# Optimization experiments

Measured on AMD Instinct MI355X. Metric: run time of the kernel, lower is better.

The kernel has to match this reference:

```python
import jax, jax.numpy as jnp
import numpy as np

RADIUS = 4.0
NS = 4      # num_samples
SUB = 2     # subsampling

def sqdist(a, b):
    # a [B,M,3], b [B,N,3] -> squared dists [B,M,N]
    return jnp.sum((a[:, :, None, :] - b[:, None, :, :]) ** 2, axis=-1)

def furthest_point_sample(xyz, npoint):
    # xyz [B,N,3] -> idx [B,npoint]; matches CUDA FPS (starts at index 0)
    B, N, _ = xyz.shape
    barange = jnp.arange(B)
    def step(carry, _):
        dists, last = carry
        lastp = xyz[barange, last][:, None, :]          # [B,1,3]
        d = jnp.sum((xyz - lastp) ** 2, axis=-1)        # [B,N]
        dists = jnp.minimum(dists, d)
        nxt = jnp.argmax(dists, axis=1).astype(jnp.int32)
        return (dists, nxt), last
    init = (jnp.full((B, N), 1e10, xyz.dtype), jnp.zeros((B,), jnp.int32))
    _, idxs = jax.lax.scan(step, init, None, length=npoint)
    return jnp.transpose(idxs)                          # [B,npoint]

def gather_points(xyz, idx):
    # xyz [B,N,3], idx [B,M] -> [B,M,3]
    return jax.vmap(lambda x, i: x[i])(xyz, idx)

def group(features, idx):
    # features [B,C,N], idx [B,M,S] -> [B,C,M,S]
    return jax.vmap(lambda f, i: f[:, i])(features, idx)

def ball_query(radius, nsample, xyz, new_xyz):
    # first nsample points of xyz (by index order) within radius of each center,
    # slots padded with the first found neighbor (0 if none) - CUDA ball_query semantics
    N = xyz.shape[1]
    d2 = sqdist(new_xyz, xyz)                                  # [B,M,N]
    order = jnp.where(d2 < radius * radius, jnp.arange(N)[None, None, :], N)
    idx = jnp.sort(order, axis=-1)[..., :nsample]
    first = idx[..., :1]
    idx = jnp.where(idx == N, first, idx)
    return jnp.where(idx == N, 0, idx).astype(jnp.int32)

def point_rnn_cell(P1, X1, state, W, radius, nsample, out_ch):
    # P1 [B,M,3]; X1 [B,Cin,M] or None; W [Cout, Cin+Cout+3]
    B, M, _ = P1.shape
    if state is None:
        P2 = jnp.zeros((B, M, 3), P1.dtype)
        S2 = jnp.zeros((B, out_ch, M), P1.dtype)
    else:
        P2, S2 = state
    idx = ball_query(radius, nsample, P2, P1)                  # [B,M,S]
    P2g = group(jnp.transpose(P2, (0, 2, 1)), idx)             # [B,3,M,S]
    S2g = group(S2, idx)                                       # [B,Cout,M,S]
    disp = P2g - jnp.transpose(P1, (0, 2, 1))[..., None]
    if X1 is None:
        corr = jnp.concatenate([S2g, disp], axis=1)
    else:
        X1e = jnp.broadcast_to(X1[..., None], X1.shape + (nsample,))
        corr = jnp.concatenate([S2g, X1e, disp], axis=1)
    S1 = jnp.max(jnp.einsum('oc,bcms->boms', W, corr), axis=3)  # 1x1 conv, no bias, then max-pool
    return (P1, S1)

def query_group_max(radius, nsample, xyz, new_xyz, features):
    # QueryAndGroup(use_xyz=False) followed by max over neighbors
    idx = ball_query(radius, nsample, xyz, new_xyz)
    return jnp.max(group(features, idx), axis=-1)              # [B,C,M]

def three_interpolate(unknown, known, known_feats):
    # 3-NN inverse-(squared)-distance interpolation; PointnetFPModule(mlp=[128]) has no conv layers
    d2 = sqdist(unknown, known)                                # [B,n,m]
    negd, idx = jax.lax.top_k(-d2, 3)                          # 3 smallest squared dists
    recip = 1.0 / (-negd + 1e-8)
    w = recip / jnp.sum(recip, axis=-1, keepdims=True)         # [B,n,3]
    gf = group(known_feats, idx)                               # [B,C,n,3]
    return jnp.sum(gf * w[:, None, :, :], axis=-1)             # [B,C,n]

def run_step(frame, states, W1, W2, W3, N):
    N1, N2, N3 = N // SUB, N // SUB ** 2, N // SUB ** 3
    xyz1 = gather_points(frame, furthest_point_sample(frame, N1))
    s1 = point_rnn_cell(xyz1, None, states[0], W1, 1 * RADIUS + 1e-6, 3 * NS, 64)
    xyz2 = gather_points(s1[0], furthest_point_sample(s1[0], N2))
    feat2 = query_group_max(2 * RADIUS / 4 + 1e-6, NS, s1[0], xyz2, s1[1])
    s2 = point_rnn_cell(xyz2, feat2, states[1], W2, 2 * RADIUS + 1e-6, 2 * NS, 128)
    xyz3 = gather_points(s2[0], furthest_point_sample(s2[0], N3))
    feat3 = query_group_max(4 * RADIUS / 4 + 1e-6, NS, s2[0], xyz3, s2[1])
    s3 = point_rnn_cell(xyz3, feat3, states[2], W3, 3 * RADIUS + 1e-6, 1 * NS, 256)
    return (s1, s2, s3)

def setup_inputs() -> dict:
    key = jax.random.key(0)
    ks = jax.random.split(key, 12)
    B, L, N = 4, 8, 2048
    sc = 0.05
    return {
        'xyzs': jax.random.normal(ks[0], (B, L, N, 3), jnp.float32),
        'en_w1': jax.random.normal(ks[1], (64, 67), jnp.float32) * sc,
        'en_w2': jax.random.normal(ks[2], (128, 195), jnp.float32) * sc,
        'en_w3': jax.random.normal(ks[3], (256, 387), jnp.float32) * sc,
        'de_w1': jax.random.normal(ks[4], (64, 67), jnp.float32) * sc,
        'de_w2': jax.random.normal(ks[5], (128, 195), jnp.float32) * sc,
        'de_w3': jax.random.normal(ks[6], (256, 387), jnp.float32) * sc,
        'mlp_w1': jax.random.normal(ks[7], (64, 448), jnp.float32) * sc,
        'mlp_b1': jax.random.normal(ks[8], (64,), jnp.float32) * sc,
        'mlp_w2': jax.random.normal(ks[9], (3, 64), jnp.float32) * sc,
        'mlp_b2': jax.random.normal(ks[10], (3,), jnp.float32) * sc,
    }

def reference(xyzs, en_w1, en_w2, en_w3, de_w1, de_w2, de_w3, mlp_w1, mlp_b1, mlp_w2, mlp_b2):
    B, L, N, _ = xyzs.shape
    states = (None, None, None)
    # encoder over first L/2 frames
    for t in range(L // 2):
        states = run_step(xyzs[:, t], states, en_w1, en_w2, en_w3, N)
    frame = xyzs[:, L // 2 - 1]
    preds = []
    for t in range(L // 2, L):
        states = run_step(frame, states, de_w1, de_w2, de_w3, N)
        (p1, f1), (p2, f2), (p3, f3) = states
        l3 = jnp.concatenate([three_interpolate(p2, p3, f3), f2], axis=1)   # [B,384,N2]
        l2 = jnp.concatenate([three_interpolate(p1, p2, l3), f1], axis=1)   # [B,448,N1]
        l1 = three_interpolate(frame, p1, l2)                               # [B,448,N]
        h = jax.nn.relu(jnp.einsum('oc,bcn->bon', mlp_w1, l1) + mlp_b1[None, :, None])
        motion = jnp.einsum('oc,bcn->bon', mlp_w2, h) + mlp_b2[None, :, None]
        motion = jnp.transpose(motion, (0, 2, 1))                           # [B,N,3]
        frame = frame + motion
        preds.append(frame)
    return jnp.stack(preds, axis=1)                                          # [B,L/2,N,3]
```

## Files before the change

kernel.cpp:

```cpp
#include <hip/hip_runtime.h>

static constexpr int B  = 4;
static constexpr int N0 = 2048;
static constexpr int LF = 8;
static constexpr int M1 = 1024, M2 = 512, M3 = 256;
static constexpr int O1 = 64, O2 = 128, O3 = 256;
static constexpr int NS1 = 12, NS2 = 8, NS3 = 4, NSQ = 4;
static constexpr int C1 = 67, C2 = 195, C3 = 387;
static constexpr int C41 = 68, C42 = 196, C43 = 388;
static constexpr long XS = 3 * (long)M1;

static constexpr int WP_E1 = 0;
static constexpr int WP_E2 = 4352;
static constexpr int WP_E3 = 29440;
static constexpr int WP_D1 = 128768;
static constexpr int WP_D2 = 133120;
static constexpr int WP_D3 = 158208;
static constexpr int WP_M1 = 257536;
static constexpr int WP_TOT = 286208;

__device__ __forceinline__ float sq3(float ax, float ay, float az,
                                     float bx, float by, float bz) {
  float dx = __fsub_rn(ax, bx), dy = __fsub_rn(ay, by), dz = __fsub_rn(az, bz);
  return __fadd_rn(__fadd_rn(__fmul_rn(dx, dx), __fmul_rn(dy, dy)),
                   __fmul_rn(dz, dz));
}

template <int CTRL>
__device__ __forceinline__ int dpp_i(int v) {
  return __builtin_amdgcn_update_dpp(v, v, CTRL, 0xf, 0xf, false);
}
template <int CTRL>
__device__ __forceinline__ float dpp_maxf(float m) {
  const float o = __uint_as_float((unsigned)dpp_i<CTRL>((int)__float_as_uint(m)));
  return fmaxf(m, o);
}
template <int CTRL>
__device__ __forceinline__ unsigned dpp_minu(unsigned v) {
  const unsigned o = (unsigned)dpp_i<CTRL>((int)v);
  return o < v ? o : v;
}
template <int CTRL>
__device__ __forceinline__ void dpp_min64_step(unsigned& hi, unsigned& lo) {
  const unsigned ohi = (unsigned)dpp_i<CTRL>((int)hi);
  const unsigned olo = (unsigned)dpp_i<CTRL>((int)lo);
  const bool take = (ohi < hi) || (ohi == hi && olo < lo);
  hi = take ? ohi : hi;
  lo = take ? olo : lo;
}

__device__ __forceinline__ float4 wsum3(float4 a, float4 b, float4 c,
                                        float w0, float w1, float w2) {
  float4 r;
  r.x = __fadd_rn(__fadd_rn(__fmul_rn(a.x, w0), __fmul_rn(b.x, w1)), __fmul_rn(c.x, w2));
  r.y = __fadd_rn(__fadd_rn(__fmul_rn(a.y, w0), __fmul_rn(b.y, w1)), __fmul_rn(c.y, w2));
  r.z = __fadd_rn(__fadd_rn(__fmul_rn(a.z, w0), __fmul_rn(b.z, w1)), __fmul_rn(c.z, w2));
  r.w = __fadd_rn(__fadd_rn(__fmul_rn(a.w, w0), __fmul_rn(b.w, w1)), __fmul_rn(c.w, w2));
  return r;
}

__global__ __launch_bounds__(256) void pack_w(
    const float* __restrict__ e1, const float* __restrict__ e2,
    const float* __restrict__ e3, const float* __restrict__ d1,
    const float* __restrict__ d2, const float* __restrict__ d3,
    const float* __restrict__ m1, float* __restrict__ dst) {
  int t = blockIdx.x * 256 + threadIdx.x;
  const float* src; int C, O; long dof;
  if (t < 4288) { src = e1; C = C1; O = O1; dof = WP_E1; }
  else if (t < 29248) { src = e2; C = C2; O = O2; dof = WP_E2; t -= 4288; }
  else if (t < 128320) { src = e3; C = C3; O = O3; dof = WP_E3; t -= 29248; }
  else if (t < 132608) { src = d1; C = C1; O = O1; dof = WP_D1; t -= 128320; }
  else if (t < 157568) { src = d2; C = C2; O = O2; dof = WP_D2; t -= 132608; }
  else if (t < 256640) { src = d3; C = C3; O = O3; dof = WP_D3; t -= 157568; }
  else if (t < 285312) { src = m1; C = 448; O = 64; dof = WP_M1; t -= 256640; }
  else return;
  const int o = t / C, c = t - o * C;
  dst[dof + ((long)(c >> 2) * O + o) * 4 + (c & 3)] = src[t];
}

template <int N, int NPOINT>
__global__ __launch_bounds__(256, 1) void fps8(const float* __restrict__ pts,
                                               long s1, long s2,
                                               float* __restrict__ out,
                                               long o1, long o2,
                                               const float* __restrict__ cfsrc,
                                               float* __restrict__ cfdst,
                                               int copy_y) {
  if ((int)blockIdx.y == copy_y) {
    const int b = blockIdx.x;
    for (int e = threadIdx.x; e < N0 * 3; e += 256)
      cfdst[(long)b * N0 * 3 + e] = cfsrc[((long)b * LF + (LF / 2 - 1)) * N0 * 3 + e];
    return;
  }
  constexpr int K = N / 256;
  const float* p = pts + (long)blockIdx.x * s1 + (long)blockIdx.y * s2;
  float* outb = out + (long)blockIdx.x * o1 + (long)blockIdx.y * o2;
  const int tid = threadIdx.x;
  const int lane = tid & 63;
  const int wid = tid >> 6;
  __shared__ float4 sp[N];
  __shared__ float sel[NPOINT * 3];
  __shared__ unsigned long long wbest[2][4];
  float ppx[K], ppy[K], ppz[K], dist[K];
#pragma unroll
  for (int k = 0; k < K; ++k) {
    const int j = k * 256 + tid;
    const float x = p[3 * j + 0], y = p[3 * j + 1], z = p[3 * j + 2];
    ppx[k] = x; ppy[k] = y; ppz[k] = z;
    sp[j] = make_float4(x, y, z, 0.f);
    dist[k] = 1e10f;
  }
  __syncthreads();
  const float4 c0 = sp[0];
  float lx = c0.x, ly = c0.y, lz = c0.z;
  for (int i = 0; i < NPOINT; ++i) {
    if (tid == 0) {
      sel[3 * i + 0] = lx; sel[3 * i + 1] = ly; sel[3 * i + 2] = lz;
    }
    float bdm = 0.f;
    int bk = 0;
#pragma unroll
    for (int k = 0; k < K; ++k) {
      const float d = sq3(ppx[k], ppy[k], ppz[k], lx, ly, lz);
      const float dm = fminf(dist[k], d);
      dist[k] = dm;
      const bool take = dm > bdm;
      bdm = take ? dm : bdm;
      bk = take ? k : bk;
    }
    float mx = bdm;
    mx = dpp_maxf<0x111>(mx);
    mx = dpp_maxf<0x112>(mx);
    mx = dpp_maxf<0x114>(mx);
    mx = dpp_maxf<0x118>(mx);
    mx = dpp_maxf<0x142>(mx);
    mx = dpp_maxf<0x143>(mx);
    const float wmax = __uint_as_float(
        (unsigned)__builtin_amdgcn_readlane((int)__float_as_uint(mx), 63));
    unsigned cand = (bdm == wmax) ? (unsigned)((bk << 8) + tid) : 0xFFFFFFFFu;
    cand = dpp_minu<0x111>(cand);
    cand = dpp_minu<0x112>(cand);
    cand = dpp_minu<0x114>(cand);
    cand = dpp_minu<0x118>(cand);
    cand = dpp_minu<0x142>(cand);
    cand = dpp_minu<0x143>(cand);
    const unsigned minj = (unsigned)__builtin_amdgcn_readlane((int)cand, 63);
    if (lane == 63)
      wbest[i & 1][wid] =
          ((unsigned long long)__float_as_uint(wmax) << 32) | (2047u - minj);
    __syncthreads();
    unsigned long long gk = 0ull;
#pragma unroll
    for (int w = 0; w < 4; ++w) {
      const unsigned long long e = wbest[i & 1][w];
      gk = (e > gk) ? e : gk;
    }
    const int gidx = 2047 - (int)(gk & 0x7FFull);
    const float4 c = sp[gidx];
    lx = c.x; ly = c.y; lz = c.z;
  }
  __syncthreads();
  for (int e = tid; e < NPOINT * 3; e += 256) outb[e] = sel[e];
}

template <int NS>
__device__ __forceinline__ void wave_bq(float qx, float qy, float qz,
                                        const float* __restrict__ src, int Ns,
                                        float r2, int* __restrict__ sidx, int lane) {
  int cnt = 0;
  for (int base = 0; base < Ns && cnt < NS; base += 64) {
    const int j = base + lane;
    bool in = false;
    if (j < Ns)
      in = sq3(qx, qy, qz, src[3 * j], src[3 * j + 1], src[3 * j + 2]) < r2;
    const unsigned long long mask = __ballot(in);
    const int pos = cnt + (int)__popcll(mask & ((1ull << lane) - 1ull));
    if (in && pos < NS) sidx[pos] = j;
    cnt += (int)__popcll(mask);
  }
  const int cc = cnt < NS ? cnt : NS;
  const int fill = (cc > 0) ? sidx[0] : 0;
  if (lane >= cc && lane < NS) sidx[lane] = fill;
}

struct FusedArgs {
  int n1, n2, n3, nk;
  const float *c1_xc, *c1_xp, *c1_W, *c1_Sp; float* c1_Sc;
  const float *c2_xc, *c2_xp, *c2_W, *c2_Sp, *c2_S1; float* c2_Sc;
  const float *c3_xc, *c3_xp, *c3_W, *c3_Sp, *c3_S2; float* c3_Sc;
  const float *k_xc, *k_frame;
  int *ii2, *ii1, *ii0;
  float *iw2, *iw1, *iw0;
  float r2c1, r2c2, r2q2, r2c3, r2q3;
};

__global__ __launch_bounds__(256) void fused_cells(FusedArgs a) {
  __shared__ __align__(16) float smem[3312];
  const int tid = threadIdx.x;
  const int lane = tid & 63;
  const int wave = tid >> 6;
  int bid = blockIdx.x;

  if (bid < a.n1) {
    float* corr2 = smem + (size_t)wave * 828;
    int* sidx = (int*)(corr2 + 816);
    const int u = bid * 4 + wave;
    const int b = u >> 10, m = u & (M1 - 1);
    const float* p1 = a.c1_xc + (long)b * XS + 3 * m;
    const float p1x = p1[0], p1y = p1[1], p1z = p1[2];
    const float* p2b = a.c1_xp + (long)b * XS;
    wave_bq<NS1>(p1x, p1y, p1z, p2b, M1, a.r2c1, sidx, lane);
    __builtin_amdgcn_wave_barrier();
    for (int e = lane; e < NS1 * C41; e += 64) {
      const int s = e / C41, c = e - s * C41;
      const int j = sidx[s];
      float v;
      if (c < O1) {
        v = a.c1_Sp[((long)b * M1 + j) * O1 + c];
      } else if (c < C1) {
        const int d = c - O1;
        v = __fsub_rn(p2b[3 * j + d], (d == 0) ? p1x : ((d == 1) ? p1y : p1z));
      } else {
        v = 0.f;
      }
      corr2[e] = v;
    }
    __builtin_amdgcn_wave_barrier();
    const float4* wp4 = (const float4*)a.c1_W;
    float accs[NS1];
#pragma unroll
    for (int s = 0; s < NS1; ++s) accs[s] = 0.f;
    for (int q = 0; q < C41 / 4; ++q) {
      const float4 wv = wp4[(long)q * O1 + lane];
#pragma unroll
      for (int s = 0; s < NS1; ++s) {
        const float4 cv = *(const float4*)(corr2 + s * C41 + 4 * q);
        float acc = accs[s];
        acc = fmaf(wv.x, cv.x, acc);
        acc = fmaf(wv.y, cv.y, acc);
        acc = fmaf(wv.z, cv.z, acc);
        acc = fmaf(wv.w, cv.w, acc);
        accs[s] = acc;
      }
    }
    float best = accs[0];
#pragma unroll
    for (int s = 1; s < NS1; ++s) best = fmaxf(best, accs[s]);
    a.c1_Sc[((long)b * M1 + m) * O1 + lane] = best;
    return;
  }
  bid -= a.n1;

  if (bid < a.n2) {
    const int half = tid >> 7;
    const int ht = tid & 127;
    const int hw = (tid >> 6) & 1;
    float* base = smem + (size_t)half * 1644;
    float* corr2 = base;
    int* sidx = (int*)(base + 1568);
    int* sfidx = (int*)(base + 1576);
    float* feat = base + 1580;
    const int u = bid * 2 + half;
    const int b = u >> 9, m = u & (M2 - 1);
    const float* p1 = a.c2_xc + (long)b * XS + 3 * m;
    const float p1x = p1[0], p1y = p1[1], p1z = p1[2];
    const float* p2b = a.c2_xp + (long)b * XS;
    if (hw == 0)
      wave_bq<NS2>(p1x, p1y, p1z, p2b, M2, a.r2c2, sidx, lane);
    else
      wave_bq<NSQ>(p1x, p1y, p1z, a.c2_xc + (long)b * XS, M1, a.r2q2, sfidx, lane);
    __syncthreads();
    if (ht < O1) {
      float bv = -3.0e38f;
#pragma unroll
      for (int s = 0; s < NSQ; ++s)
        bv = fmaxf(bv, a.c2_S1[((long)b * M1 + sfidx[s]) * O1 + ht]);
      feat[ht] = bv;
    }
    __syncthreads();
    for (int e = ht; e < NS2 * C42; e += 128) {
      const int s = e / C42, c = e - s * C42;
      const int j = sidx[s];
      float v;
      if (c < O2) {
        v = a.c2_Sp[((long)b * M2 + j) * O2 + c];
      } else if (c < O2 + O1) {
        v = feat[c - O2];
      } else if (c < C2) {
        const int d = c - O2 - O1;
        v = __fsub_rn(p2b[3 * j + d], (d == 0) ? p1x : ((d == 1) ? p1y : p1z));
      } else {
        v = 0.f;
      }
      corr2[e] = v;
    }
    __syncthreads();
    const float4* wp4 = (const float4*)a.c2_W;
    float accs[NS2];
#pragma unroll
    for (int s = 0; s < NS2; ++s) accs[s] = 0.f;
    for (int q = 0; q < C42 / 4; ++q) {
      const float4 wv = wp4[(long)q * O2 + ht];
#pragma unroll
      for (int s = 0; s < NS2; ++s) {
        const float4 cv = *(const float4*)(corr2 + s * C42 + 4 * q);
        float acc = accs[s];
        acc = fmaf(wv.x, cv.x, acc);
        acc = fmaf(wv.y, cv.y, acc);
        acc = fmaf(wv.z, cv.z, acc);
        acc = fmaf(wv.w, cv.w, acc);
        accs[s] = acc;
      }
    }
    float best = accs[0];
#pragma unroll
    for (int s = 1; s < NS2; ++s) best = fmaxf(best, accs[s]);
    a.c2_Sc[((long)b * M2 + m) * O2 + ht] = best;
    return;
  }
  bid -= a.n2;

  if (bid < a.n3) {
    float* corr2 = smem;
    int* sidx = (int*)(smem + 1552);
    int* sfidx = (int*)(smem + 1556);
    float* feat = smem + 1560;
    const int b = bid >> 8, m = bid & (M3 - 1);
    const float* p1 = a.c3_xc + (long)b * XS + 3 * m;
    const float p1x = p1[0], p1y = p1[1], p1z = p1[2];
    const float* p2b = a.c3_xp + (long)b * XS;
    if (wave == 0)
      wave_bq<NS3>(p1x, p1y, p1z, p2b, M3, a.r2c3, sidx, lane);
    else if (wave == 1)
      wave_bq<NSQ>(p1x, p1y, p1z, a.c3_xc + (long)b * XS, M2, a.r2q3, sfidx, lane);
    __syncthreads();
    if (tid < O2) {
      float bv = -3.0e38f;
#pragma unroll
      for (int s = 0; s < NSQ; ++s)
        bv = fmaxf(bv, a.c3_S2[((long)b * M2 + sfidx[s]) * O2 + tid]);
      feat[tid] = bv;
    }
    __syncthreads();
    for (int e = tid; e < NS3 * C43; e += 256) {
      const int s = e / C43, c = e - s * C43;
      const int j = sidx[s];
      float v;
      if (c < O3) {
        v = a.c3_Sp[((long)b * M3 + j) * O3 + c];
      } else if (c < O3 + O2) {
        v = feat[c - O3];
      } else if (c < C3) {
        const int d = c - O3 - O2;
        v = __fsub_rn(p2b[3 * j + d], (d == 0) ? p1x : ((d == 1) ? p1y : p1z));
      } else {
        v = 0.f;
      }
      corr2[e] = v;
    }
    __syncthreads();
    const float4* wp4 = (const float4*)a.c3_W;
    float accs[NS3];
#pragma unroll
    for (int s = 0; s < NS3; ++s) accs[s] = 0.f;
    for (int q = 0; q < C43 / 4; ++q) {
      const float4 wv = wp4[(long)q * O3 + tid];
#pragma unroll
      for (int s = 0; s < NS3; ++s) {
        const float4 cv = *(const float4*)(corr2 + s * C43 + 4 * q);
        float acc = accs[s];
        acc = fmaf(wv.x, cv.x, acc);
        acc = fmaf(wv.y, cv.y, acc);
        acc = fmaf(wv.z, cv.z, acc);
        acc = fmaf(wv.w, cv.w, acc);
        accs[s] = acc;
      }
    }
    float best = accs[0];
#pragma unroll
    for (int s = 1; s < NS3; ++s) best = fmaxf(best, accs[s]);
    a.c3_Sc[((long)b * M3 + m) * O3 + tid] = best;
    return;
  }
  bid -= a.n3;

  {
    int q, Mu, Mk;
    const float* unk; long ustr; int* oi; float* ow;
    if (bid < 512) {
      q = bid * 4 + wave; Mu = M2; Mk = M3; unk = a.k_xc; ustr = XS;
      oi = a.ii2; ow = a.iw2;
    } else if (bid < 1536) {
      q = (bid - 512) * 4 + wave; Mu = M1; Mk = M2; unk = a.k_xc; ustr = XS;
      oi = a.ii1; ow = a.iw1;
    } else {
      q = (bid - 1536) * 4 + wave; Mu = N0; Mk = M1; unk = a.k_frame; ustr = 3L * N0;
      oi = a.ii0; ow = a.iw0;
    }
    const int b = q / Mu, m = q - b * Mu;
    const float* qq = unk + (long)b * ustr + (long)m * 3;
    const float qx = qq[0], qy = qq[1], qz = qq[2];
    const float* s = a.k_xc + (long)b * XS;
    unsigned long long k0 = ~0ull, k1 = ~0ull, k2 = ~0ull;
    const int steps = Mk >> 6;
    for (int t7 = 0; t7 < steps; ++t7) {
      const int j = (t7 << 6) + lane;
      const float dd = sq3(qx, qy, qz, s[3 * j], s[3 * j + 1], s[3 * j + 2]);
      const unsigned long long key =
          ((unsigned long long)__float_as_uint(dd) << 32) | (unsigned)j;
      if (key < k0) { k2 = k1; k1 = k0; k0 = key; }
      else if (key < k1) { k2 = k1; k1 = key; }
      else if (key < k2) { k2 = key; }
    }
    float dw[3]; int jw[3];
#pragma unroll
    for (int r = 0; r < 3; ++r) {
      unsigned mhi = (unsigned)(k0 >> 32), mlo = (unsigned)k0;
      dpp_min64_step<0x111>(mhi, mlo);
      dpp_min64_step<0x112>(mhi, mlo);
      dpp_min64_step<0x114>(mhi, mlo);
      dpp_min64_step<0x118>(mhi, mlo);
      dpp_min64_step<0x142>(mhi, mlo);
      dpp_min64_step<0x143>(mhi, mlo);
      const unsigned whi = (unsigned)__builtin_amdgcn_readlane((int)mhi, 63);
      const unsigned wlo = (unsigned)__builtin_amdgcn_readlane((int)mlo, 63);
      const unsigned long long w = ((unsigned long long)whi << 32) | wlo;
      dw[r] = __uint_as_float(whi);
      jw[r] = (int)wlo;
      if (k0 == w) { k0 = k1; k1 = k2; k2 = ~0ull; }
    }
    const float r0 = 1.0f / __fadd_rn(dw[0], 1e-8f);
    const float r1 = 1.0f / __fadd_rn(dw[1], 1e-8f);
    const float r2 = 1.0f / __fadd_rn(dw[2], 1e-8f);
    const float sum = __fadd_rn(__fadd_rn(r0, r1), r2);
    if (lane == 0) {
      ow[q * 3 + 0] = r0 / sum;
      ow[q * 3 + 1] = r1 / sum;
      ow[q * 3 + 2] = r2 / sum;
      oi[q * 3 + 0] = jw[0];
      oi[q * 3 + 1] = jw[1];
      oi[q * 3 + 2] = jw[2];
    }
  }
}

__global__ __launch_bounds__(256) void buildl2_kernel(const float* __restrict__ S3c,
                                                      const float* __restrict__ S2c,
                                                      const float* __restrict__ S1c,
                                                      const int* __restrict__ ii1,
                                                      const float* __restrict__ iw1,
                                                      const int* __restrict__ ii2,
                                                      const float* __restrict__ iw2,
                                                      float* __restrict__ l2) {
  const int t = blockIdx.x * 256 + threadIdx.x;
  const int bm = t / 112;
  const int c0 = (t - bm * 112) * 4;
  const int b = bm >> 10;
  const int* id1 = ii1 + (long)bm * 3;
  const float* w1 = iw1 + (long)bm * 3;
  float4 v;
  if (c0 < O3) {
    float4 v2[3];
#pragma unroll
    for (int k = 0; k < 3; ++k) {
      const int m2 = id1[k];
      const int* id2 = ii2 + ((long)b * M2 + m2) * 3;
      const float* w2 = iw2 + ((long)b * M2 + m2) * 3;
      const float4 s0 = *(const float4*)(S3c + ((long)b * M3 + id2[0]) * O3 + c0);
      const float4 s1 = *(const float4*)(S3c + ((long)b * M3 + id2[1]) * O3 + c0);
      const float4 s2 = *(const float4*)(S3c + ((long)b * M3 + id2[2]) * O3 + c0);
      v2[k] = wsum3(s0, s1, s2, w2[0], w2[1], w2[2]);
    }
    v = wsum3(v2[0], v2[1], v2[2], w1[0], w1[1], w1[2]);
  } else if (c0 < 384) {
    const int cc = c0 - O3;
    const float4 s0 = *(const float4*)(S2c + ((long)b * M2 + id1[0]) * O2 + cc);
    const float4 s1 = *(const float4*)(S2c + ((long)b * M2 + id1[1]) * O2 + cc);
    const float4 s2 = *(const float4*)(S2c + ((long)b * M2 + id1[2]) * O2 + cc);
    v = wsum3(s0, s1, s2, w1[0], w1[1], w1[2]);
  } else {
    v = *(const float4*)(S1c + (long)bm * O1 + (c0 - 384));
  }
  *(float4*)(l2 + (long)bm * 448 + c0) = v;
}

__global__ __launch_bounds__(256) void mlp_kernel(const float* __restrict__ l2,
                                                  const int* __restrict__ ii,
                                                  const float* __restrict__ iw,
                                                  const float* __restrict__ W1P,
                                                  const float* __restrict__ b1,
                                                  const float* __restrict__ W2,
                                                  const float* __restrict__ b2,
                                                  float* __restrict__ frame,
                                                  float* __restrict__ out, int td) {
  __shared__ __align__(16) float smem[4 * 512];
  const int lane = threadIdx.x & 63;
  const int wave = threadIdx.x >> 6;
  float* col = smem + (size_t)wave * 512;
  float* h = col + 448;
  const int u = blockIdx.x * 4 + wave;
  const int b = u >> 11, n = u & (N0 - 1);
  const int* id = ii + (long)u * 3;
  const float* w = iw + (long)u * 3;
  const float w0 = w[0], w1 = w[1], w2v = w[2];
  const float4* r0 = (const float4*)(l2 + ((long)b * M1 + id[0]) * 448);
  const float4* r1 = (const float4*)(l2 + ((long)b * M1 + id[1]) * 448);
  const float4* r2 = (const float4*)(l2 + ((long)b * M1 + id[2]) * 448);
  float4* col4 = (float4*)col;
  for (int q = lane; q < 112; q += 64)
    col4[q] = wsum3(r0[q], r1[q], r2[q], w0, w1, w2v);
  __builtin_amdgcn_wave_barrier();
  const float4* wp4 = (const float4*)W1P;
  float acc = b1[lane];
  for (int q = 0; q < 112; ++q) {
    const float4 wv = wp4[(long)q * 64 + lane];
    const float4 cv = col4[q];
    acc = fmaf(wv.x, cv.x, acc);
    acc = fmaf(wv.y, cv.y, acc);
    acc = fmaf(wv.z, cv.z, acc);
    acc = fmaf(wv.w, cv.w, acc);
  }
  h[lane] = fmaxf(acc, 0.0f);
  __builtin_amdgcn_wave_barrier();
  if (lane < 3) {
    const float* w2r = W2 + lane * 64;
    float acc2 = b2[lane];
    for (int c = 0; c < 64; ++c) acc2 = fmaf(w2r[c], h[c], acc2);
    const float nf = frame[(long)u * 3 + lane] + acc2;
    frame[(long)u * 3 + lane] = nf;
    out[(((long)b * 4 + td) * N0 + n) * 3 + lane] = nf;
  }
}

extern "C" void kernel_launch(void* const* d_in, const int* in_sizes, int n_in,
                              void* d_out, int out_size, void* d_ws, size_t ws_size,
                              hipStream_t stream) {
  const float* xyzs = (const float*)d_in[0];
  const float* enw[3] = {(const float*)d_in[1], (const float*)d_in[2], (const float*)d_in[3]};
  const float* dew[3] = {(const float*)d_in[4], (const float*)d_in[5], (const float*)d_in[6]};
  const float* mw1 = (const float*)d_in[7];
  const float* mb1 = (const float*)d_in[8];
  const float* mw2 = (const float*)d_in[9];
  const float* mb2 = (const float*)d_in[10];
  float* out = (float*)d_out;

  float* ws = (float*)d_ws;
  size_t off = 0;
  auto alloc = [&](size_t nn) { float* p = ws + off; off += nn; return p; };
  const long st1 = (long)B * M1 * 3;
  float* frame = alloc((size_t)B * N0 * 3);
  float* xyz1e = alloc((size_t)4 * st1);
  float* xyz1d[2] = {alloc((size_t)st1), alloc((size_t)st1)};
  float* z1 = alloc((size_t)st1);
  float* S1bf[2] = {alloc((size_t)B * O1 * M1), alloc((size_t)B * O1 * M1)};
  float* S2bf[2] = {alloc((size_t)B * O2 * M2), alloc((size_t)B * O2 * M2)};
  float* S3bf[2] = {alloc((size_t)B * O3 * M3), alloc((size_t)B * O3 * M3)};
  float* l2 = alloc((size_t)B * 448 * M1);
  float* iw0 = alloc((size_t)B * N0 * 3);
  int* ii0 = (int*)alloc((size_t)B * N0 * 3);
  float* iw1 = alloc((size_t)B * M1 * 3);
  int* ii1 = (int*)alloc((size_t)B * M1 * 3);
  float* iw2 = alloc((size_t)B * M2 * 3);
  int* ii2 = (int*)alloc((size_t)B * M2 * 3);
  float* wt = alloc((size_t)WP_TOT);

  hipMemsetAsync(z1, 0, (size_t)st1 * 4, stream);
  hipMemsetAsync(S1bf[1], 0, (size_t)B * O1 * M1 * 4, stream);
  hipMemsetAsync(S2bf[1], 0, (size_t)B * O2 * M2 * 4, stream);
  hipMemsetAsync(S3bf[1], 0, (size_t)B * O3 * M3 * 4, stream);
  hipMemsetAsync(wt, 0, (size_t)WP_TOT * 4, stream);

  double r;
  r = 4.0 + 1e-6;             const float r2c1 = (float)(r * r);
  r = 2.0 * 4.0 / 4.0 + 1e-6; const float r2q2 = (float)(r * r);
  r = 2.0 * 4.0 + 1e-6;       const float r2c2 = (float)(r * r);
  r = 4.0 * 4.0 / 4.0 + 1e-6; const float r2q3 = (float)(r * r);
  r = 3.0 * 4.0 + 1e-6;       const float r2c3 = (float)(r * r);

  pack_w<<<dim3((285312 + 255) / 256), 256, 0, stream>>>(
      enw[0], enw[1], enw[2], dew[0], dew[1], dew[2], mw1, wt);

  fps8<2048, 1024><<<dim3(B, 5), 256, 0, stream>>>(xyzs, (long)LF * N0 * 3,
                                                   (long)N0 * 3, xyz1e, XS, st1,
                                                   xyzs, frame, 4);

  const float* x1_of_t[LF] = {
      xyz1e + 0 * st1, xyz1e + 1 * st1, xyz1e + 2 * st1, xyz1e + 3 * st1,
      xyz1e + 3 * st1, xyz1d[0], xyz1d[1], xyz1d[0]};

  const float* wp1[2] = {wt + WP_E1, wt + WP_D1};
  const float* wp2[2] = {wt + WP_E2, wt + WP_D2};
  const float* wp3[2] = {wt + WP_E3, wt + WP_D3};

  auto launch_fused = [&](int t1, int t2, int t3, int tk) {
    FusedArgs a{};
    int nb = 0;
    if (t1 >= 0) {
      a.n1 = B * M1 / 4;
      a.c1_xc = x1_of_t[t1];
      a.c1_xp = (t1 == 0) ? z1 : x1_of_t[t1 - 1];
      a.c1_W = wp1[t1 >= 4];
      a.c1_Sp = S1bf[1 - (t1 & 1)];
      a.c1_Sc = S1bf[t1 & 1];
      nb += a.n1;
    }
    if (t2 >= 0) {
      a.n2 = B * M2 / 2;
      a.c2_xc = x1_of_t[t2];
      a.c2_xp = (t2 == 0) ? z1 : x1_of_t[t2 - 1];
      a.c2_W = wp2[t2 >= 4];
      a.c2_Sp = S2bf[1 - (t2 & 1)];
      a.c2_S1 = S1bf[t2 & 1];
      a.c2_Sc = S2bf[t2 & 1];
      nb += a.n2;
    }
    if (t3 >= 0) {
      a.n3 = B * M3;
      a.c3_xc = x1_of_t[t3];
      a.c3_xp = (t3 == 0) ? z1 : x1_of_t[t3 - 1];
      a.c3_W = wp3[t3 >= 4];
      a.c3_Sp = S3bf[1 - (t3 & 1)];
      a.c3_S2 = S2bf[t3 & 1];
      a.c3_Sc = S3bf[t3 & 1];
      nb += a.n3;
    }
    if (tk >= 0) {
      a.nk = 3584;
      a.k_xc = x1_of_t[tk];
      a.k_frame = frame;
      a.ii2 = ii2; a.ii1 = ii1; a.ii0 = ii0;
      a.iw2 = iw2; a.iw1 = iw1; a.iw0 = iw0;
      nb += a.nk;
    }
    a.r2c1 = r2c1; a.r2c2 = r2c2; a.r2q2 = r2q2; a.r2c3 = r2c3; a.r2q3 = r2q3;
    fused_cells<<<dim3((unsigned)nb), 256, 0, stream>>>(a);
  };

  auto tail = [&](int t) {
    buildl2_kernel<<<dim3(B * M1 * 112 / 256), 256, 0, stream>>>(
        S3bf[t & 1], S2bf[t & 1], S1bf[t & 1], ii1, iw1, ii2, iw2, l2);
    mlp_kernel<<<dim3(B * N0 / 4), 256, 0, stream>>>(
        l2, ii0, iw0, wt + WP_M1, mb1, mw2, mb2, frame, out, t - 4);
  };

  launch_fused(0, -1, -1, -1);
  launch_fused(1, 0, -1, -1);
  launch_fused(2, 1, 0, -1);
  launch_fused(3, 2, 1, -1);
  launch_fused(4, 3, 2, 4);
  launch_fused(-1, 4, 3, -1);
  launch_fused(-1, -1, 4, -1);
  tail(4);

  for (int t = 5; t < LF; ++t) {
    fps8<2048, 1024><<<dim3(B, 1), 256, 0, stream>>>(frame, (long)N0 * 3, 0,
                                                     (float*)x1_of_t[t], XS, 0,
                                                     nullptr, nullptr, -1);
    launch_fused(t, -1, -1, t);
    launch_fused(-1, t, -1, -1);
    launch_fused(-1, -1, t, -1);
    tail(t);
  }
  (void)in_sizes; (void)n_in; (void)out_size; (void)ws_size;
}
```

Before: 2.775 ms.

## Select two FPS points per iteration using top-3 candidate speculation

Rewrites furthest point sampling so each iteration keeps a per-thread top-3 of (distance, index) keys, reduces them across waves, and when the second candidate stays farther than the third after accounting for distance to the first pick, commits both points in one round. This aims to halve the number of block-wide barriers and serial reduction rounds in the FPS loop, which is latency-bound. In exchange each round does more work: a 64-bit three-pass DPP reduction, a top-3 insertion per element and a cross-wave merge. The exactness argument depends on the top-3 test matching sequential argmax with its tie-breaking, so results could drift.

```diff
diff --git a/kernel.cpp b/kernel.cpp
--- a/kernel.cpp
+++ b/kernel.cpp
@@ -31,14 +31,12 @@
   return __builtin_amdgcn_update_dpp(v, v, CTRL, 0xf, 0xf, false);
 }
 template <int CTRL>
-__device__ __forceinline__ float dpp_maxf(float m) {
-  const float o = __uint_as_float((unsigned)dpp_i<CTRL>((int)__float_as_uint(m)));
-  return fmaxf(m, o);
-}
-template <int CTRL>
-__device__ __forceinline__ unsigned dpp_minu(unsigned v) {
-  const unsigned o = (unsigned)dpp_i<CTRL>((int)v);
-  return o < v ? o : v;
+__device__ __forceinline__ void dpp_max_step(unsigned& hi, unsigned& lo) {
+  const unsigned ohi = (unsigned)dpp_i<CTRL>((int)hi);
+  const unsigned olo = (unsigned)dpp_i<CTRL>((int)lo);
+  const bool take = (ohi > hi) || (ohi == hi && olo > lo);
+  hi = take ? ohi : hi;
+  lo = take ? olo : lo;
 }
 template <int CTRL>
 __device__ __forceinline__ void dpp_min64_step(unsigned& hi, unsigned& lo) {
@@ -79,7 +77,7 @@
 }
 
 template <int N, int NPOINT>
-__global__ __launch_bounds__(256, 1) void fps8(const float* __restrict__ pts,
+__global__ __launch_bounds__(256, 1) void fps9(const float* __restrict__ pts,
                                                long s1, long s2,
                                                float* __restrict__ out,
                                                long o1, long o2,
@@ -100,7 +98,7 @@
   const int wid = tid >> 6;
   __shared__ float4 sp[N];
   __shared__ float sel[NPOINT * 3];
-  __shared__ unsigned long long wbest[2][4];
+  __shared__ unsigned long long wsl[2][4][3];
   float ppx[K], ppy[K], ppz[K], dist[K];
 #pragma unroll
   for (int k = 0; k < K; ++k) {
@@ -112,52 +110,104 @@
   }
   __syncthreads();
   const float4 c0 = sp[0];
-  float lx = c0.x, ly = c0.y, lz = c0.z;
-  for (int i = 0; i < NPOINT; ++i) {
+  float p1x = c0.x, p1y = c0.y, p1z = c0.z;
+  float p2x = c0.x, p2y = c0.y, p2z = c0.z;
+  int pend2 = 0;
+  int cnt = 0, r = 0;
+  while (true) {
     if (tid == 0) {
-      sel[3 * i + 0] = lx; sel[3 * i + 1] = ly; sel[3 * i + 2] = lz;
-    }
-    float bdm = 0.f;
-    int bk = 0;
-#pragma unroll
-    for (int k = 0; k < K; ++k) {
-      const float d = sq3(ppx[k], ppy[k], ppz[k], lx, ly, lz);
-      const float dm = fminf(dist[k], d);
-      dist[k] = dm;
-      const bool take = dm > bdm;
-      bdm = take ? dm : bdm;
-      bk = take ? k : bk;
-    }
-    float mx = bdm;
-    mx = dpp_maxf<0x111>(mx);
-    mx = dpp_maxf<0x112>(mx);
-    mx = dpp_maxf<0x114>(mx);
-    mx = dpp_maxf<0x118>(mx);
-    mx = dpp_maxf<0x142>(mx);
-    mx = dpp_maxf<0x143>(mx);
-    const float wmax = __uint_as_float(
-        (unsigned)__builtin_amdgcn_readlane((int)__float_as_uint(mx), 63));
-    unsigned cand = (bdm == wmax) ? (unsigned)((bk << 8) + tid) : 0xFFFFFFFFu;
-    cand = dpp_minu<0x111>(cand);
-    cand = dpp_minu<0x112>(cand);
-    cand = dpp_minu<0x114>(cand);
-    cand = dpp_minu<0x118>(cand);
-    cand = dpp_minu<0x142>(cand);
-    cand = dpp_minu<0x143>(cand);
-    const unsigned minj = (unsigned)__builtin_amdgcn_readlane((int)cand, 63);
-    if (lane == 63)
-      wbest[i & 1][wid] =
-          ((unsigned long long)__float_as_uint(wmax) << 32) | (2047u - minj);
+      sel[3 * cnt + 0] = p1x; sel[3 * cnt + 1] = p1y; sel[3 * cnt + 2] = p1z;
+      if (pend2) {
+        sel[3 * cnt + 3] = p2x; sel[3 * cnt + 4] = p2y; sel[3 * cnt + 5] = p2z;
+      }
+    }
+    cnt += 1 + pend2;
+    if (cnt >= NPOINT) break;
+    unsigned long long K0 = 0ull, K1 = 0ull, K2 = 0ull;
+    if (pend2) {
+#pragma unroll
+      for (int k = 0; k < K; ++k) {
+        const float d1 = sq3(ppx[k], ppy[k], ppz[k], p1x, p1y, p1z);
+        float dm = fminf(dist[k], d1);
+        const float d2 = sq3(ppx[k], ppy[k], ppz[k], p2x, p2y, p2z);
+        dm = fminf(dm, d2);
+        dist[k] = dm;
+        const unsigned long long key =
+            ((unsigned long long)__float_as_uint(dm) << 32) |
+            (unsigned)(2047 - (k * 256 + tid));
+        if (key > K0) { K2 = K1; K1 = K0; K0 = key; }
+        else if (key > K1) { K2 = K1; K1 = key; }
+        else if (key > K2) { K2 = key; }
+      }
+    } else {
+#pragma unroll
+      for (int k = 0; k < K; ++k) {
+        const float d1 = sq3(ppx[k], ppy[k], ppz[k], p1x, p1y, p1z);
+        const float dm = fminf(dist[k], d1);
+        dist[k] = dm;
+        const unsigned long long key =
+            ((unsigned long long)__float_as_uint(dm) << 32) |
+            (unsigned)(2047 - (k * 256 + tid));
+        if (key > K0) { K2 = K1; K1 = K0; K0 = key; }
+        else if (key > K1) { K2 = K1; K1 = key; }
+        else if (key > K2) { K2 = key; }
+      }
+    }
+    unsigned long long wv0, wv1, wv2;
+#pragma unroll
+    for (int e = 0; e < 3; ++e) {
+      unsigned hi = (unsigned)(K0 >> 32), lo = (unsigned)K0;
+      dpp_max_step<0x111>(hi, lo);
+      dpp_max_step<0x112>(hi, lo);
+      dpp_max_step<0x114>(hi, lo);
+      dpp_max_step<0x118>(hi, lo);
+      dpp_max_step<0x142>(hi, lo);
+      dpp_max_step<0x143>(hi, lo);
+      const unsigned whi = (unsigned)__builtin_amdgcn_readlane((int)hi, 63);
+      const unsigned wlo = (unsigned)__builtin_amdgcn_readlane((int)lo, 63);
+      const unsigned long long wm = ((unsigned long long)whi << 32) | wlo;
+      if (e == 0) wv0 = wm; else if (e == 1) wv1 = wm; else wv2 = wm;
+      if (K0 == wm) { K0 = K1; K1 = K2; K2 = 0ull; }
+    }
+    if (lane == 63) {
+      wsl[r & 1][wid][0] = wv0;
+      wsl[r & 1][wid][1] = wv1;
+      wsl[r & 1][wid][2] = wv2;
+    }
     __syncthreads();
-    unsigned long long gk = 0ull;
-#pragma unroll
-    for (int w = 0; w < 4; ++w) {
-      const unsigned long long e = wbest[i & 1][w];
-      gk = (e > gk) ? e : gk;
-    }
-    const int gidx = 2047 - (int)(gk & 0x7FFull);
-    const float4 c = sp[gidx];
-    lx = c.x; ly = c.y; lz = c.z;
+    unsigned long long t00 = wsl[r & 1][0][0], t01 = wsl[r & 1][0][1], t02 = wsl[r & 1][0][2];
+    unsigned long long t10 = wsl[r & 1][1][0], t11 = wsl[r & 1][1][1], t12 = wsl[r & 1][1][2];
+    unsigned long long t20 = wsl[r & 1][2][0], t21 = wsl[r & 1][2][1], t22 = wsl[r & 1][2][2];
+    unsigned long long t30 = wsl[r & 1][3][0], t31 = wsl[r & 1][3][1], t32 = wsl[r & 1][3][2];
+    int l0 = 0, l1 = 0, l2 = 0, l3 = 0;
+    unsigned long long G0, G1, G2;
+#pragma unroll
+    for (int pass = 0; pass < 3; ++pass) {
+      const unsigned long long h0 = (l0 == 0) ? t00 : (l0 == 1) ? t01 : (l0 == 2) ? t02 : 0ull;
+      const unsigned long long h1 = (l1 == 0) ? t10 : (l1 == 1) ? t11 : (l1 == 2) ? t12 : 0ull;
+      const unsigned long long h2 = (l2 == 0) ? t20 : (l2 == 1) ? t21 : (l2 == 2) ? t22 : 0ull;
+      const unsigned long long h3 = (l3 == 0) ? t30 : (l3 == 1) ? t31 : (l3 == 2) ? t32 : 0ull;
+      const unsigned long long m01 = h0 > h1 ? h0 : h1;
+      const unsigned long long m23 = h2 > h3 ? h2 : h3;
+      const unsigned long long g = m01 > m23 ? m01 : m23;
+      if (pass == 0) G0 = g; else if (pass == 1) G1 = g; else G2 = g;
+      l0 += (h0 == g); l1 += (h1 == g); l2 += (h2 == g); l3 += (h3 == g);
+    }
+    const int g1 = 2047 - (int)(G0 & 0x7FFull);
+    const int g2 = 2047 - (int)(G1 & 0x7FFull);
+    const float4 cc1 = sp[g1];
+    const float4 cc2 = sp[g2];
+    const float v2 = __uint_as_float((unsigned)(G1 >> 32));
+    const float v3 = __uint_as_float((unsigned)(G2 >> 32));
+    const float d21 = sq3(cc2.x, cc2.y, cc2.z, cc1.x, cc1.y, cc1.z);
+    const float v2p = fminf(v2, d21);
+    const bool take2 = (v2p > v3) && (cnt + 2 <= NPOINT);
+    p1x = cc1.x; p1y = cc1.y; p1z = cc1.z;
+    p2x = take2 ? cc2.x : cc1.x;
+    p2y = take2 ? cc2.y : cc1.y;
+    p2z = take2 ? cc2.z : cc1.z;
+    pend2 = take2 ? 1 : 0;
+    ++r;
   }
   __syncthreads();
   for (int e = tid; e < NPOINT * 3; e += 256) outb[e] = sel[e];
@@ -580,7 +630,7 @@
   pack_w<<<dim3((285312 + 255) / 256), 256, 0, stream>>>(
       enw[0], enw[1], enw[2], dew[0], dew[1], dew[2], mw1, wt);
 
-  fps8<2048, 1024><<<dim3(B, 5), 256, 0, stream>>>(xyzs, (long)LF * N0 * 3,
+  fps9<2048, 1024><<<dim3(B, 5), 256, 0, stream>>>(xyzs, (long)LF * N0 * 3,
                                                    (long)N0 * 3, xyz1e, XS, st1,
                                                    xyzs, frame, 4);
 
@@ -653,7 +703,7 @@
   tail(4);
 
   for (int t = 5; t < LF; ++t) {
-    fps8<2048, 1024><<<dim3(B, 1), 256, 0, stream>>>(frame, (long)N0 * 3, 0,
+    fps9<2048, 1024><<<dim3(B, 1), 256, 0, stream>>>(frame, (long)N0 * 3, 0,
                                                      (float*)x1_of_t[t], XS, 0,
                                                      nullptr, nullptr, -1);
     launch_fused(t, -1, -1, t);
```

After: 4.332 ms. +56.1%, slower.

## Run furthest point sampling in a single wavefront to drop block barriers

Applied to the files above, without the earlier changes.

The FPS kernel now uses one 64-lane wavefront per block, so each lane holds 32 points in registers, and the per-iteration cross-wave reduction through shared memory and __syncthreads is removed. The argmax index is carried directly as the global point index and reduced with DPP min, so no 64-bit key packing is needed. This trades four-wave parallelism on the distance update for the removal of 1024 block barriers per sample, and raises register pressure. The frame-copy path is also vectorized to float4.

```diff
diff --git a/kernel.cpp b/kernel.cpp
--- a/kernel.cpp
+++ b/kernel.cpp
@@ -79,7 +79,7 @@
 }
 
 template <int N, int NPOINT>
-__global__ __launch_bounds__(256, 1) void fps8(const float* __restrict__ pts,
+__global__ __launch_bounds__(64, 1) void fps10(const float* __restrict__ pts,
                                                long s1, long s2,
                                                float* __restrict__ out,
                                                long o1, long o2,
@@ -88,37 +88,34 @@
                                                int copy_y) {
   if ((int)blockIdx.y == copy_y) {
     const int b = blockIdx.x;
-    for (int e = threadIdx.x; e < N0 * 3; e += 256)
-      cfdst[(long)b * N0 * 3 + e] = cfsrc[((long)b * LF + (LF / 2 - 1)) * N0 * 3 + e];
+    const float4* s4 = (const float4*)(cfsrc + ((long)b * LF + (LF / 2 - 1)) * N0 * 3);
+    float4* d4 = (float4*)(cfdst + (long)b * N0 * 3);
+    for (int e = threadIdx.x; e < N0 * 3 / 4; e += 64) d4[e] = s4[e];
     return;
   }
-  constexpr int K = N / 256;
+  constexpr int K = N / 64;
   const float* p = pts + (long)blockIdx.x * s1 + (long)blockIdx.y * s2;
   float* outb = out + (long)blockIdx.x * o1 + (long)blockIdx.y * o2;
-  const int tid = threadIdx.x;
-  const int lane = tid & 63;
-  const int wid = tid >> 6;
+  const int lane = threadIdx.x;
   __shared__ float4 sp[N];
   __shared__ float sel[NPOINT * 3];
-  __shared__ unsigned long long wbest[2][4];
   float ppx[K], ppy[K], ppz[K], dist[K];
 #pragma unroll
   for (int k = 0; k < K; ++k) {
-    const int j = k * 256 + tid;
+    const int j = k * 64 + lane;
     const float x = p[3 * j + 0], y = p[3 * j + 1], z = p[3 * j + 2];
     ppx[k] = x; ppy[k] = y; ppz[k] = z;
     sp[j] = make_float4(x, y, z, 0.f);
     dist[k] = 1e10f;
   }
-  __syncthreads();
   const float4 c0 = sp[0];
   float lx = c0.x, ly = c0.y, lz = c0.z;
   for (int i = 0; i < NPOINT; ++i) {
-    if (tid == 0) {
+    if (lane == 0) {
       sel[3 * i + 0] = lx; sel[3 * i + 1] = ly; sel[3 * i + 2] = lz;
     }
     float bdm = 0.f;
-    int bk = 0;
+    int bj = 0;
 #pragma unroll
     for (int k = 0; k < K; ++k) {
       const float d = sq3(ppx[k], ppy[k], ppz[k], lx, ly, lz);
@@ -126,7 +123,7 @@
       dist[k] = dm;
       const bool take = dm > bdm;
       bdm = take ? dm : bdm;
-      bk = take ? k : bk;
+      bj = take ? (k * 64 + lane) : bj;
     }
     float mx = bdm;
     mx = dpp_maxf<0x111>(mx);
@@ -137,30 +134,18 @@
     mx = dpp_maxf<0x143>(mx);
     const float wmax = __uint_as_float(
         (unsigned)__builtin_amdgcn_readlane((int)__float_as_uint(mx), 63));
-    unsigned cand = (bdm == wmax) ? (unsigned)((bk << 8) + tid) : 0xFFFFFFFFu;
+    unsigned cand = (bdm == wmax) ? (unsigned)bj : 0xFFFFFFFFu;
     cand = dpp_minu<0x111>(cand);
     cand = dpp_minu<0x112>(cand);
     cand = dpp_minu<0x114>(cand);
     cand = dpp_minu<0x118>(cand);
     cand = dpp_minu<0x142>(cand);
     cand = dpp_minu<0x143>(cand);
-    const unsigned minj = (unsigned)__builtin_amdgcn_readlane((int)cand, 63);
-    if (lane == 63)
-      wbest[i & 1][wid] =
-          ((unsigned long long)__float_as_uint(wmax) << 32) | (2047u - minj);
-    __syncthreads();
-    unsigned long long gk = 0ull;
-#pragma unroll
-    for (int w = 0; w < 4; ++w) {
-      const unsigned long long e = wbest[i & 1][w];
-      gk = (e > gk) ? e : gk;
-    }
-    const int gidx = 2047 - (int)(gk & 0x7FFull);
-    const float4 c = sp[gidx];
+    const int minj = __builtin_amdgcn_readlane((int)cand, 63);
+    const float4 c = sp[minj];
     lx = c.x; ly = c.y; lz = c.z;
   }
-  __syncthreads();
-  for (int e = tid; e < NPOINT * 3; e += 256) outb[e] = sel[e];
+  for (int e = lane; e < NPOINT * 3; e += 64) outb[e] = sel[e];
 }
 
 template <int NS>
@@ -580,7 +565,7 @@
   pack_w<<<dim3((285312 + 255) / 256), 256, 0, stream>>>(
       enw[0], enw[1], enw[2], dew[0], dew[1], dew[2], mw1, wt);
 
-  fps8<2048, 1024><<<dim3(B, 5), 256, 0, stream>>>(xyzs, (long)LF * N0 * 3,
+  fps10<2048, 1024><<<dim3(B, 5), 64, 0, stream>>>(xyzs, (long)LF * N0 * 3,
                                                    (long)N0 * 3, xyz1e, XS, st1,
                                                    xyzs, frame, 4);
 
@@ -653,7 +638,7 @@
   tail(4);
 
   for (int t = 5; t < LF; ++t) {
-    fps8<2048, 1024><<<dim3(B, 1), 256, 0, stream>>>(frame, (long)N0 * 3, 0,
+    fps10<2048, 1024><<<dim3(B, 1), 64, 0, stream>>>(frame, (long)N0 * 3, 0,
                                                      (float*)x1_of_t[t], XS, 0,
                                                      nullptr, nullptr, -1);
     launch_fused(t, -1, -1, t);
```

Result: slower. 4.495 ms (+62.0%).
